# Kernel tuning notes

Measured on AMD Instinct MI355X. Metric: run time of the kernel, lower is better.

## Reference

```python
import jax, jax.numpy as jnp
import numpy as np

T, N, F_IN, H1, H2, F_OUT = 48, 4096, 64, 64, 32, 64

def setup_inputs() -> dict:
    key = jax.random.key(0)
    ks = jax.random.split(key, 14)
    sc = 0.05
    x = jax.random.normal(ks[0], (T, N, F_IN), jnp.float32)
    adj = jax.random.uniform(ks[1], (N, N), jnp.float32) / N  # roughly row-normalized dense adjacency
    fc_w = jax.random.normal(ks[2], (F_IN, H1), jnp.float32) * sc
    fc_b = jnp.zeros((H1,), jnp.float32)
    Wz = jax.random.normal(ks[3], (H1, F_OUT), jnp.float32) * sc
    Wr = jax.random.normal(ks[4], (H1, F_OUT), jnp.float32) * sc
    Wh = jax.random.normal(ks[5], (H1, F_OUT), jnp.float32) * sc
    Lz = jax.random.normal(ks[6], (2 * F_OUT, F_OUT), jnp.float32) * sc
    Lr = jax.random.normal(ks[7], (2 * F_OUT, F_OUT), jnp.float32) * sc
    Lh = jax.random.normal(ks[8], (2 * F_OUT, F_OUT), jnp.float32) * sc
    bz = jnp.zeros((F_OUT,), jnp.float32)
    br = jnp.zeros((F_OUT,), jnp.float32)
    bh = jnp.zeros((F_OUT,), jnp.float32)
    return {"x": x, "adj": adj, "fc_w": fc_w, "fc_b": fc_b,
            "Wz": Wz, "Wr": Wr, "Wh": Wh,
            "Lz": Lz, "Lr": Lr, "Lh": Lh,
            "bz": bz, "br": br, "bh": bh}

def reference(x, adj, fc_w, fc_b, Wz, Wr, Wh, Lz, Lr, Lh, bz, br, bh):
    # relu(fc(x)) followed by relu(unsqueeze) == single relu
    xh = jax.nn.relu(x @ fc_w + fc_b)          # [T, N, H1]
    h0 = jnp.zeros((N, F_OUT), x.dtype)

    def step(h, xi):
        # TGCN cell: dense graph conv A @ (X W) feeding GRU-style gates
        az = adj @ (xi @ Wz)                   # [N, F_OUT]
        ar = adj @ (xi @ Wr)
        ah = adj @ (xi @ Wh)
        z = jax.nn.sigmoid(jnp.concatenate([az, h], axis=-1) @ Lz + bz)
        r = jax.nn.sigmoid(jnp.concatenate([ar, h], axis=-1) @ Lr + br)
        h_tilde = jnp.tanh(jnp.concatenate([ah, h * r], axis=-1) @ Lh + bh)
        h_new = z * h + (1.0 - z) * h_tilde
        return h_new, None

    h, _ = jax.lax.scan(step, h0, xh)
    return h[None]                              # [1, N, F_OUT]
```

## Files before the change

### kernel.cpp

```cpp
#include <hip/hip_runtime.h>

typedef unsigned short u16;
typedef unsigned char u8;
typedef short s16x8 __attribute__((ext_vector_type(8)));
typedef unsigned short u16x4 __attribute__((ext_vector_type(4)));
typedef float f32x4 __attribute__((ext_vector_type(4)));

#define AS1 __attribute__((address_space(1)))
#define AS3 __attribute__((address_space(3)))

__device__ __forceinline__ void g2l16(const void* g, void* l) {
  __builtin_amdgcn_global_load_lds((const AS1 void*)g, (AS3 void*)l, 16, 0, 0);
}

__device__ __forceinline__ float b2f(u16 u) {
  union { unsigned int i; float f; } x; x.i = ((unsigned int)u) << 16; return x.f;
}
__device__ __forceinline__ u16 f2b(float f) {
  unsigned int u = __builtin_bit_cast(unsigned int, f);
  return (u16)((u + 0x7fffu + ((u >> 16) & 1u)) >> 16);
}
__device__ __forceinline__ u8 f2e4m3(float v) {
  int p = __builtin_amdgcn_cvt_pk_fp8_f32(v, 0.f, 0, false);
  return (u8)(p & 0xff);
}
__device__ __forceinline__ float sigm(float x) { return 1.f / (1.f + __expf(-x)); }
__device__ __forceinline__ float tanh_f(float x) { return 2.f / (1.f + __expf(-2.f * x)) - 1.f; }


__global__ __launch_bounds__(256) void kcvt(const float* __restrict__ a, u8* __restrict__ ab) {
  size_t idx = (size_t)blockIdx.x * 256 + threadIdx.x;
  const float4* src = (const float4*)a;
  uint4 o;
  unsigned int r[4];
#pragma unroll
  for (int k = 0; k < 4; ++k) {
    float4 v = src[idx * 4 + k];
    unsigned int p = __builtin_amdgcn_cvt_pk_fp8_f32(v.x * 4096.f, v.y * 4096.f, 0, false);
    p = __builtin_amdgcn_cvt_pk_fp8_f32(v.z * 4096.f, v.w * 4096.f, p, true);
    r[k] = p;
  }
  o.x = r[0]; o.y = r[1]; o.z = r[2]; o.w = r[3];
  ((uint4*)ab)[idx] = o;
}

__global__ __launch_bounds__(256) void k0(
    const float* __restrict__ fcw,
    const float* __restrict__ Wz, const float* __restrict__ Wr, const float* __restrict__ Wh,
    const float* __restrict__ Lz, const float* __restrict__ Lr, const float* __restrict__ Lh,
    u16* __restrict__ fcwT, u16* __restrict__ wct, u16* __restrict__ lbt) {
  int b = blockIdx.x, t = threadIdx.x;
  if (b < 48) {
    int idx = b * 256 + t;
    int c_cat = idx >> 6, hh = idx & 63;
    int g = c_cat >> 6, c = c_cat & 63;
    const float* W = (g == 0) ? Wz : (g == 1) ? Wr : Wh;
    const float* L = (g == 0) ? Lz : (g == 1) ? Lr : Lh;
    float acc = 0.f;
    for (int m = 0; m < 64; ++m) acc += W[hh * 64 + m] * L[m * 64 + c];
    wct[c_cat * 64 + hh] = f2b(acc);
  } else if (b == 48) {
    for (int i = 0; i < 16; ++i) {
      int idx = t * 16 + i; int hh = idx >> 6, f = idx & 63;
      fcwT[hh * 64 + f] = f2b(fcw[f * 64 + hh]);
    }
  } else {
    int g = b - 49;
    const float* L = (g == 0) ? Lz : (g == 1) ? Lr : Lh;
    for (int i = 0; i < 16; ++i) {
      int idx = t * 16 + i; int c = idx >> 6, hh = idx & 63;
      lbt[g * 4096 + c * 64 + hh] = f2b(L[(64 + hh) * 64 + c]);
    }
  }
}

__global__ __launch_bounds__(256) void k1(
    const float* __restrict__ x, const float* __restrict__ fcb,
    const u16* __restrict__ fcwT, u8* __restrict__ xht) {
  __shared__ __align__(16) u16 xs[128 * 72];
  __shared__ __align__(16) u16 fw[64 * 72];
  __shared__ float fb[64];
  int tid = threadIdx.x, w = tid >> 6, l = tid & 63;
  int t = blockIdx.y, n0 = blockIdx.x * 128;
#pragma unroll
  for (int i2 = 0; i2 < 2; ++i2) {
    int g = tid + 256 * i2;
    s16x8 v = *(const s16x8*)&fcwT[g * 8];
    *(s16x8*)&fw[(g >> 3) * 72 + (g & 7) * 8] = v;
  }
  const float4* xg = (const float4*)(x + ((size_t)t * 4096 + n0) * 64);
#pragma unroll
  for (int i = 0; i < 8; ++i) {
    int s = tid * 8 + i;
    float4 v = xg[s];
    u16x4 p; p[0] = f2b(v.x); p[1] = f2b(v.y); p[2] = f2b(v.z); p[3] = f2b(v.w);
    *(u16x4*)&xs[(s >> 4) * 72 + (s & 15) * 4] = p;
  }
  if (tid < 64) fb[tid] = fcb[tid];
  __syncthreads();

  int lm = l & 15, q = l >> 4;
  f32x4 acc[4][2];
#pragma unroll
  for (int i = 0; i < 4; ++i)
#pragma unroll
    for (int j = 0; j < 2; ++j)
#pragma unroll
      for (int r = 0; r < 4; ++r) acc[i][j][r] = 0.f;
#pragma unroll
  for (int s = 0; s < 2; ++s) {
    s16x8 af[4], bf[2];
#pragma unroll
    for (int i = 0; i < 4; ++i) af[i] = *(const s16x8*)&fw[(16 * i + lm) * 72 + 32 * s + q * 8];
#pragma unroll
    for (int j = 0; j < 2; ++j) bf[j] = *(const s16x8*)&xs[(32 * w + 16 * j + lm) * 72 + 32 * s + q * 8];
#pragma unroll
    for (int i = 0; i < 4; ++i)
#pragma unroll
      for (int j = 0; j < 2; ++j)
        acc[i][j] = __builtin_amdgcn_mfma_f32_16x16x32_bf16(af[i], bf[j], acc[i][j], 0, 0, 0);
  }
#pragma unroll
  for (int i = 0; i < 4; ++i)
#pragma unroll
    for (int j = 0; j < 2; ++j)
#pragma unroll
      for (int r = 0; r < 4; ++r) {
        int h = 16 * i + q * 4 + r;
        int node = 32 * w + 16 * j + lm;
        float v = acc[i][j][r] + fb[h];
        xht[(size_t)(t * 64 + h) * 4096 + n0 + node] = f2e4m3(v > 0.f ? v : 0.f);
      }
}

__global__ __launch_bounds__(256) void k2(
    const u8* __restrict__ A, const u8* __restrict__ B, u16* __restrict__ M) {
  __shared__ __align__(16) u8 As[128 * 128];
  __shared__ __align__(16) u8 Bs[128 * 128];
  int tid = threadIdx.x, w = tid >> 6, l = tid & 63;
  int nt = blockIdx.x, mt = blockIdx.y;
  const u8* Ab = A + (size_t)mt * 128 * 4096;
  const u8* Bb = B + (size_t)nt * 128 * 4096;
  int lm = l & 15, q = l >> 4;
  int wm = w >> 1, wn = w & 1;
  int srow = l >> 3;
  int scol = ((l & 7) ^ srow) * 16;
  f32x4 acc[4][4];
#pragma unroll
  for (int i = 0; i < 4; ++i)
#pragma unroll
    for (int j = 0; j < 4; ++j)
#pragma unroll
      for (int r = 0; r < 4; ++r) acc[i][j][r] = 0.f;
  for (int k0b = 0; k0b < 4096; k0b += 128) {
#pragma unroll
    for (int j = 0; j < 4; ++j) {
      int r0 = w * 32 + j * 8;
      g2l16(Ab + (size_t)(r0 + srow) * 4096 + k0b + scol, (char*)As + r0 * 128);
      g2l16(Bb + (size_t)(r0 + srow) * 4096 + k0b + scol, (char*)Bs + r0 * 128);
    }
    __syncthreads();
#pragma unroll
    for (int s = 0; s < 4; ++s) {
      int ch = 2 * s + (q >> 1), sub = (q & 1) * 8;
      long af[4], bf[4];
#pragma unroll
      for (int i = 0; i < 4; ++i) {
        int row = 64 * wm + 16 * i + lm;
        af[i] = *(const long*)&As[row * 128 + (ch ^ (row & 7)) * 16 + sub];
      }
#pragma unroll
      for (int j = 0; j < 4; ++j) {
        int row = 64 * wn + 16 * j + lm;
        bf[j] = *(const long*)&Bs[row * 128 + (ch ^ (row & 7)) * 16 + sub];
      }
#pragma unroll
      for (int i = 0; i < 4; ++i)
#pragma unroll
        for (int j = 0; j < 4; ++j)
          acc[i][j] = __builtin_amdgcn_mfma_f32_16x16x32_fp8_fp8(af[i], bf[j], acc[i][j], 0, 0, 0);
    }
    __syncthreads();
  }
  const float sc = 1.f / 4096.f;
#pragma unroll
  for (int i = 0; i < 4; ++i)
#pragma unroll
    for (int j = 0; j < 4; ++j)
#pragma unroll
      for (int r = 0; r < 4; ++r) {
        int row = mt * 128 + 64 * wm + 16 * i + q * 4 + r;
        int col = nt * 128 + 64 * wn + 16 * j + lm;
        M[(size_t)row * 3072 + col] = f2b(acc[i][j][r] * sc);
      }
}

__global__ __launch_bounds__(256) void k3(
    const u16* __restrict__ M, const u16* __restrict__ wct, const u16* __restrict__ lbt,
    const float* __restrict__ bz, const float* __restrict__ br, const float* __restrict__ bh,
    float* __restrict__ out) {
  __shared__ __align__(16) u16 hhi[16 * 72], hlo[16 * 72];
  __shared__ __align__(16) u16 rhi[16 * 72], rlo[16 * 72];
  int tid = threadIdx.x, w = tid >> 6, l = tid & 63;
  int nb0 = blockIdx.x * 16;
  int lm = l & 15, q = l >> 4;
  int cb = 16 * w + q * 4;
  s16x8 afw[3][2], afl[3][2];
#pragma unroll
  for (int g = 0; g < 3; ++g)
#pragma unroll
    for (int s = 0; s < 2; ++s) {
      afw[g][s] = *(const s16x8*)&wct[(size_t)(g * 64 + 16 * w + lm) * 64 + 32 * s + q * 8];
      afl[g][s] = *(const s16x8*)&lbt[(size_t)(g * 64 + 16 * w + lm) * 64 + 32 * s + q * 8];
    }
  for (int i = tid; i < 16 * 72; i += 256) { hhi[i] = 0; hlo[i] = 0; }
  f32x4 bzv, brv, bhv, hv;
#pragma unroll
  for (int r = 0; r < 4; ++r) {
    bzv[r] = bz[cb + r]; brv[r] = br[cb + r]; bhv[r] = bh[cb + r]; hv[r] = 0.f;
  }
  __syncthreads();

  const u16* Mrow = M + (size_t)(nb0 + lm) * 3072;
  s16x8 Mn[2];
  Mn[0] = *(const s16x8*)&Mrow[q * 8];
  Mn[1] = *(const s16x8*)&Mrow[32 + q * 8];

  for (int t = 0; t < 48; ++t) {
    s16x8 Mc[2] = {Mn[0], Mn[1]};
    if (t < 47) {
      Mn[0] = *(const s16x8*)&Mrow[(t + 1) * 64 + q * 8];
      Mn[1] = *(const s16x8*)&Mrow[(t + 1) * 64 + 32 + q * 8];
    }
    f32x4 uz, ur;
#pragma unroll
    for (int r = 0; r < 4; ++r) { uz[r] = 0.f; ur[r] = 0.f; }
#pragma unroll
    for (int s = 0; s < 2; ++s) {
      s16x8 hh = *(const s16x8*)&hhi[lm * 72 + 32 * s + q * 8];
      s16x8 hl = *(const s16x8*)&hlo[lm * 72 + 32 * s + q * 8];
      uz = __builtin_amdgcn_mfma_f32_16x16x32_bf16(afw[0][s], Mc[s], uz, 0, 0, 0);
      uz = __builtin_amdgcn_mfma_f32_16x16x32_bf16(afl[0][s], hh, uz, 0, 0, 0);
      uz = __builtin_amdgcn_mfma_f32_16x16x32_bf16(afl[0][s], hl, uz, 0, 0, 0);
      ur = __builtin_amdgcn_mfma_f32_16x16x32_bf16(afw[1][s], Mc[s], ur, 0, 0, 0);
      ur = __builtin_amdgcn_mfma_f32_16x16x32_bf16(afl[1][s], hh, ur, 0, 0, 0);
      ur = __builtin_amdgcn_mfma_f32_16x16x32_bf16(afl[1][s], hl, ur, 0, 0, 0);
    }
    f32x4 zv, rv;
#pragma unroll
    for (int r = 0; r < 4; ++r) {
      zv[r] = sigm(uz[r] + bzv[r]);
      rv[r] = sigm(ur[r] + brv[r]);
    }
    {
      u16x4 phi, plo;
#pragma unroll
      for (int r = 0; r < 4; ++r) {
        float p = hv[r] * rv[r];
        u16 hi = f2b(p); phi[r] = hi; plo[r] = f2b(p - b2f(hi));
      }
      *(u16x4*)&rhi[lm * 72 + cb] = phi;
      *(u16x4*)&rlo[lm * 72 + cb] = plo;
    }
    __syncthreads();
    f32x4 uh;
#pragma unroll
    for (int r = 0; r < 4; ++r) uh[r] = 0.f;
#pragma unroll
    for (int s = 0; s < 2; ++s) {
      s16x8 rh = *(const s16x8*)&rhi[lm * 72 + 32 * s + q * 8];
      s16x8 rl = *(const s16x8*)&rlo[lm * 72 + 32 * s + q * 8];
      uh = __builtin_amdgcn_mfma_f32_16x16x32_bf16(afw[2][s], Mc[s], uh, 0, 0, 0);
      uh = __builtin_amdgcn_mfma_f32_16x16x32_bf16(afl[2][s], rh, uh, 0, 0, 0);
      uh = __builtin_amdgcn_mfma_f32_16x16x32_bf16(afl[2][s], rl, uh, 0, 0, 0);
    }
    {
      u16x4 phi, plo;
#pragma unroll
      for (int r = 0; r < 4; ++r) {
        float th = tanh_f(uh[r] + bhv[r]);
        float hn = zv[r] * hv[r] + (1.f - zv[r]) * th;
        hv[r] = hn;
        u16 hi = f2b(hn); phi[r] = hi; plo[r] = f2b(hn - b2f(hi));
      }
      *(u16x4*)&hhi[lm * 72 + cb] = phi;
      *(u16x4*)&hlo[lm * 72 + cb] = plo;
    }
    __syncthreads();
  }
#pragma unroll
  for (int r = 0; r < 4; ++r)
    out[(size_t)(nb0 + lm) * 64 + cb + r] = hv[r];
}

extern "C" void kernel_launch(void* const* d_in, const int* in_sizes, int n_in,
                              void* d_out, int out_size, void* d_ws, size_t ws_size,
                              hipStream_t stream) {
  const float* x   = (const float*)d_in[0];
  const float* adj = (const float*)d_in[1];
  const float* fcw = (const float*)d_in[2];
  const float* fcb = (const float*)d_in[3];
  const float* Wz  = (const float*)d_in[4];
  const float* Wr  = (const float*)d_in[5];
  const float* Wh  = (const float*)d_in[6];
  const float* Lz  = (const float*)d_in[7];
  const float* Lr  = (const float*)d_in[8];
  const float* Lh  = (const float*)d_in[9];
  const float* bz  = (const float*)d_in[10];
  const float* br  = (const float*)d_in[11];
  const float* bh  = (const float*)d_in[12];
  char* ws = (char*)d_ws;
  u8*  xht  = (u8*)(ws);
  u8*  adj8 = (u8*)(ws + (size_t)12582912);
  u16* Mm   = (u16*)(ws + (size_t)29360128);
  u16* fcwT = (u16*)(ws + (size_t)54525952);
  u16* wct  = (u16*)(ws + (size_t)54534144);
  u16* lbt  = (u16*)(ws + (size_t)54558720);
  float* outp = (float*)d_out;

  hipLaunchKernelGGL(kcvt, dim3(4096), dim3(256), 0, stream, adj, adj8);
  hipLaunchKernelGGL(k0, dim3(52), dim3(256), 0, stream,
                     fcw, Wz, Wr, Wh, Lz, Lr, Lh, fcwT, wct, lbt);
  hipLaunchKernelGGL(k1, dim3(32, 48), dim3(256), 0, stream, x, fcb, fcwT, xht);
  hipLaunchKernelGGL(k2, dim3(24, 32), dim3(256), 0, stream, adj8, xht, Mm);
  hipLaunchKernelGGL(k3, dim3(256), dim3(256), 0, stream, Mm, wct, lbt, bz, br, bh, outp);
}
```

Before: 309.6 us.

## Use scaled 16x16x128 FP8 MFMA with MFMA-native LDS layout in k2

```diff
diff --git a/kernel.cpp b/kernel.cpp
--- a/kernel.cpp
+++ b/kernel.cpp
@@ -5,6 +5,8 @@
 typedef short s16x8 __attribute__((ext_vector_type(8)));
 typedef unsigned short u16x4 __attribute__((ext_vector_type(4)));
 typedef float f32x4 __attribute__((ext_vector_type(4)));
+typedef int i32x4 __attribute__((ext_vector_type(4)));
+typedef int i32x8 __attribute__((ext_vector_type(8)));
 
 #define AS1 __attribute__((address_space(1)))
 #define AS3 __attribute__((address_space(3)))
@@ -135,16 +137,14 @@
 
 __global__ __launch_bounds__(256) void k2(
     const u8* __restrict__ A, const u8* __restrict__ B, u16* __restrict__ M) {
-  __shared__ __align__(16) u8 As[128 * 128];
-  __shared__ __align__(16) u8 Bs[128 * 128];
+  __shared__ __align__(16) u8 As[16384];
+  __shared__ __align__(16) u8 Bs[16384];
   int tid = threadIdx.x, w = tid >> 6, l = tid & 63;
   int nt = blockIdx.x, mt = blockIdx.y;
   const u8* Ab = A + (size_t)mt * 128 * 4096;
   const u8* Bb = B + (size_t)nt * 128 * 4096;
   int lm = l & 15, q = l >> 4;
   int wm = w >> 1, wn = w & 1;
-  int srow = l >> 3;
-  int scol = ((l & 7) ^ srow) * 16;
   f32x4 acc[4][4];
 #pragma unroll
   for (int i = 0; i < 4; ++i)
@@ -154,32 +154,33 @@
       for (int r = 0; r < 4; ++r) acc[i][j][r] = 0.f;
   for (int k0b = 0; k0b < 4096; k0b += 128) {
 #pragma unroll
-    for (int j = 0; j < 4; ++j) {
-      int r0 = w * 32 + j * 8;
-      g2l16(Ab + (size_t)(r0 + srow) * 4096 + k0b + scol, (char*)As + r0 * 128);
-      g2l16(Bb + (size_t)(r0 + srow) * 4096 + k0b + scol, (char*)Bs + r0 * 128);
+    for (int ri2 = 0; ri2 < 2; ++ri2) {
+      int ri = 2 * w + ri2;
+      size_t gro = (size_t)(ri * 16 + lm) * 4096 + k0b + q * 32;
+      g2l16(Ab + gro,      (char*)As + ri * 2048);
+      g2l16(Ab + gro + 16, (char*)As + ri * 2048 + 1024);
+      g2l16(Bb + gro,      (char*)Bs + ri * 2048);
+      g2l16(Bb + gro + 16, (char*)Bs + ri * 2048 + 1024);
     }
     __syncthreads();
-#pragma unroll
-    for (int s = 0; s < 4; ++s) {
-      int ch = 2 * s + (q >> 1), sub = (q & 1) * 8;
-      long af[4], bf[4];
-#pragma unroll
-      for (int i = 0; i < 4; ++i) {
-        int row = 64 * wm + 16 * i + lm;
-        af[i] = *(const long*)&As[row * 128 + (ch ^ (row & 7)) * 16 + sub];
-      }
-#pragma unroll
-      for (int j = 0; j < 4; ++j) {
-        int row = 64 * wn + 16 * j + lm;
-        bf[j] = *(const long*)&Bs[row * 128 + (ch ^ (row & 7)) * 16 + sub];
-      }
-#pragma unroll
-      for (int i = 0; i < 4; ++i)
-#pragma unroll
-        for (int j = 0; j < 4; ++j)
-          acc[i][j] = __builtin_amdgcn_mfma_f32_16x16x32_fp8_fp8(af[i], bf[j], acc[i][j], 0, 0, 0);
-    }
+    i32x8 a8[4], b8[4];
+#pragma unroll
+    for (int i = 0; i < 4; ++i) {
+      int ra = (4 * wm + i) * 2048 + l * 16;
+      i32x4 lo = *(const i32x4*)&As[ra];
+      i32x4 hi = *(const i32x4*)&As[ra + 1024];
+      a8[i] = __builtin_shufflevector(lo, hi, 0, 1, 2, 3, 4, 5, 6, 7);
+      int rb = (4 * wn + i) * 2048 + l * 16;
+      i32x4 lo2 = *(const i32x4*)&Bs[rb];
+      i32x4 hi2 = *(const i32x4*)&Bs[rb + 1024];
+      b8[i] = __builtin_shufflevector(lo2, hi2, 0, 1, 2, 3, 4, 5, 6, 7);
+    }
+#pragma unroll
+    for (int i = 0; i < 4; ++i)
+#pragma unroll
+      for (int j = 0; j < 4; ++j)
+        acc[i][j] = __builtin_amdgcn_mfma_scale_f32_16x16x128_f8f6f4(
+            a8[i], b8[j], acc[i][j], 0, 0, 0, 127, 0, 127);
     __syncthreads();
   }
   const float sc = 1.f / 4096.f;
```

Measured after the change: 321.3 us. 3.8% more time.
